# Optimization experiments

Measured on AMD Instinct MI355X. Metric: run time of the kernel, lower is better.

## Reference

```python
import jax, jax.numpy as jnp
import numpy as np


def _forward(agent_qs, ally_states, enemy_states, W_al, b_al, W_en, b_en, Wq, bq, Wk, bk,
             w1_W1, w1_b1, w1_W2, w1_b2, wf_W1, wf_b1, wf_W2, wf_b2, hb_W, hb_b,
             v_W1, v_b1, v_W2, v_b2):
    A, B, S, _ = ally_states.shape
    E = A + enemy_states.shape[0]
    D = W_al.shape[1]
    Da = Wq.shape[1]
    # entity encoders: [A,B,S,D], [En,B,S,D]
    ally_embed = ally_states @ W_al + b_al
    enemy_embed = enemy_states @ W_en + b_en
    entity = jnp.concatenate([ally_embed, enemy_embed], axis=0)      # [E,B,S,D]
    ent_bs = jnp.transpose(entity, (1, 2, 0, 3))                     # [B,S,E,D]
    q = ent_bs @ Wq + bq                                             # [B,S,E,Da]
    k = ent_bs @ Wk + bk                                             # [B,S,E,Da]
    scale = jnp.asarray(Da, q.dtype) ** 0.5
    energy = jnp.einsum('bsid,bsjd->bsij', q / scale, k)             # [B,S,E,E]
    # torch softmax(dim=1) on [BS,E,E] == softmax over the query axis i
    attn = jax.nn.softmax(energy, axis=2)
    # bmm(value[BS,D,E], attn).mean(-1) == value @ mean_j attn[:, :, e, j]
    attn_mean = jnp.mean(attn, axis=3)                               # [B,S,E]
    attn_out = jnp.einsum('bsed,bse->bsd', ent_bs, attn_mean)        # [B,S,D]
    ally_bs = jnp.transpose(ally_embed, (1, 2, 0, 3))                # [B,S,A,D]
    emi = jnp.concatenate(
        [jnp.broadcast_to(attn_out[:, :, None, :], (B, S, A, D)), ally_bs], axis=-1)  # [B,S,A,2D]
    # hypernets (2-layer)
    w1 = jnp.abs(jax.nn.relu(emi @ w1_W1 + w1_b1) @ w1_W2 + w1_b2)   # [B,S,A,M]
    b1 = attn_out @ hb_W + hb_b                                      # [B,S,M]
    hidden = jax.nn.elu(jnp.einsum('bsa,bsam->bsm', agent_qs, w1) + b1)
    wf = jnp.abs(jax.nn.relu(attn_out @ wf_W1 + wf_b1) @ wf_W2 + wf_b2)  # [B,S,M]
    v = jax.nn.relu(attn_out @ v_W1 + v_b1) @ v_W2 + v_b2            # [B,S,1]
    q_tot = jnp.einsum('bsm,bsm->bs', hidden, wf)[..., None] + v     # [B,S,1]
    return q_tot


def setup_inputs() -> dict:
    key = jax.random.key(0)
    B, S, A, En = 128, 128, 8, 8
    NFal, NFen, D, Da, M, H = 32, 16, 64, 128, 32, 64
    ks = jax.random.split(key, 32)
    p = lambda i, shape: jax.random.normal(ks[i], shape, dtype=jnp.float32) * 0.05
    return dict(
        agent_qs=jax.random.normal(ks[0], (B, S, A), dtype=jnp.float32),
        ally_states=jax.random.normal(ks[1], (A, B, S, NFal), dtype=jnp.float32),
        enemy_states=jax.random.normal(ks[2], (En, B, S, NFen), dtype=jnp.float32),
        W_al=p(3, (NFal, D)), b_al=p(4, (D,)), W_en=p(5, (NFen, D)), b_en=p(6, (D,)),
        Wq=p(7, (D, Da)), bq=p(8, (Da,)), Wk=p(9, (D, Da)), bk=p(10, (Da,)),
        w1_W1=p(11, (2 * D, H)), w1_b1=p(12, (H,)), w1_W2=p(13, (H, M)), w1_b2=p(14, (M,)),
        wf_W1=p(15, (D, H)), wf_b1=p(16, (H,)), wf_W2=p(17, (H, M)), wf_b2=p(18, (M,)),
        hb_W=p(19, (D, M)), hb_b=p(20, (M,)),
        v_W1=p(21, (D, M)), v_b1=p(22, (M,)), v_W2=p(23, (M, 1)), v_b2=p(24, (1,)),
    )


def reference(agent_qs, ally_states, enemy_states, W_al, b_al, W_en, b_en, Wq, bq, Wk, bk,
              w1_W1, w1_b1, w1_W2, w1_b2, wf_W1, wf_b1, wf_W2, wf_b2, hb_W, hb_b,
              v_W1, v_b1, v_W2, v_b2):
    return _forward(agent_qs, ally_states, enemy_states, W_al, b_al, W_en, b_en, Wq, bq, Wk, bk,
                    w1_W1, w1_b1, w1_W2, w1_b2, wf_W1, wf_b1, wf_W2, wf_b2, hb_W, hb_b,
                    v_W1, v_b1, v_W2, v_b2)
```

## Files before the change

### kernel.cpp

```cpp
#include <hip/hip_runtime.h>
#include <hip/hip_bf16.h>


#define B_   128
#define S_   128
#define BS_  (B_ * S_)
#define WPB  2
#define INV_S 0.08838834764831845f

typedef short bs8 __attribute__((ext_vector_type(8)));
typedef float f4  __attribute__((ext_vector_type(4)));

#define MFMA(a, b, c) __builtin_amdgcn_mfma_f32_16x16x32_bf16((a), (b), (c), 0, 0, 0)
#define LOADB(t) (*(const bs8*)&fb[(size_t)(t) * 512 + lane * 8])

__device__ __forceinline__ short f2bf(float f) {
    union { float f; unsigned u; } v; v.f = f;
    unsigned r = v.u + 0x7fffu + ((v.u >> 16) & 1u);
    return (short)(r >> 16);
}

__global__ __launch_bounds__(64)
void qmix_pre1(const float* __restrict__ Wq, const float* __restrict__ Wk,
               const float* __restrict__ bk,
               float* __restrict__ Ms, float* __restrict__ vq)
{
    const int blk = blockIdx.x, t = threadIdx.x;
    float p;
    if (blk < 4096) {
        const int k = blk >> 6, n = blk & 63;
        p = Wq[k * 128 + t] * Wk[n * 128 + t]
          + Wq[k * 128 + 64 + t] * Wk[n * 128 + 64 + t];
        #pragma unroll
        for (int off = 32; off >= 1; off >>= 1) p += __shfl_down(p, off, 64);
        if (t == 0) Ms[k * 64 + n] = p * INV_S;
    } else {
        const int d = blk - 4096;
        p = Wq[d * 128 + t] * bk[t] + Wq[d * 128 + 64 + t] * bk[64 + t];
        #pragma unroll
        for (int off = 32; off >= 1; off >>= 1) p += __shfl_down(p, off, 64);
        if (t == 0) vq[d] = p * INV_S;
    }
}

__global__ __launch_bounds__(64)
void qmix_pack(const float* __restrict__ Ms,
               const float* __restrict__ W_al, const float* __restrict__ W_en,
               const float* __restrict__ w1_W1, const float* __restrict__ w1_W2,
               const float* __restrict__ vq,
               short* __restrict__ fb)
{
    const int blk = blockIdx.x, lane = threadIdx.x;
    const int quad = lane >> 4, l16 = lane & 15;
    bs8 v;
    if (blk < 8) {
        const int ks = blk >> 2, n = (blk & 3) * 16 + l16;
        #pragma unroll
        for (int j = 0; j < 8; ++j)
            v[j] = f2bf(Ms[(ks * 32 + quad * 8 + j) * 64 + n]);
    } else if (blk < 16) {
        const bool en = (blk >= 12);
        const float* W = en ? W_en : W_al;
        const int Krows = en ? 16 : 32;
        const int n = ((blk - (en ? 12 : 8)) & 3) * 16 + l16;
        #pragma unroll
        for (int j = 0; j < 8; ++j) {
            const int k = quad * 8 + j;
            v[j] = (k < Krows) ? f2bf(W[k * 64 + n]) : (short)0;
        }
    } else if (blk < 32) {
        const int t = blk - 16, ks = t >> 2, n = (t & 3) * 16 + l16;
        #pragma unroll
        for (int j = 0; j < 8; ++j)
            v[j] = f2bf(w1_W1[(ks * 32 + quad * 8 + j) * 64 + n]);
    } else if (blk < 36) {
        const int t = blk - 32, ks = t >> 1, n = (t & 1) * 16 + l16;
        #pragma unroll
        for (int j = 0; j < 8; ++j)
            v[j] = f2bf(w1_W2[(ks * 32 + quad * 8 + j) * 32 + n]);
    } else {
        const int ks = blk - 36;
        #pragma unroll
        for (int j = 0; j < 8; ++j)
            v[j] = (l16 == 0) ? f2bf(vq[ks * 32 + quad * 8 + j]) : (short)0;
    }
    *(bs8*)&fb[(size_t)blk * 512 + lane * 8] = v;
}

struct __align__(16) WaveLds {
    short entb[16][72];
    short scr[16][72];
    float aoutf[64];
    short aoutb[64];
    float h[64];
    float qs[8];
};

__global__ __launch_bounds__(64 * WPB)
void qmix_main(const float* __restrict__ agent_qs,
               const float* __restrict__ ally, const float* __restrict__ enemy,
               const float* __restrict__ b_al, const float* __restrict__ b_en,
               const float* __restrict__ w1_b1, const float* __restrict__ w1_b2,
               const float* __restrict__ wf_W1, const float* __restrict__ wf_b1,
               const float* __restrict__ wf_W2, const float* __restrict__ wf_b2,
               const float* __restrict__ hb_W,  const float* __restrict__ hb_b,
               const float* __restrict__ v_W1,  const float* __restrict__ v_b1,
               const float* __restrict__ v_W2,  const float* __restrict__ v_b2,
               const short* __restrict__ fb,
               float* __restrict__ out)
{
    const int w    = threadIdx.x >> 6;
    const int lane = threadIdx.x & 63;
    const int site = blockIdx.x * WPB + w;
    const int quad = lane >> 4, l16 = lane & 15;

    __shared__ WaveLds lds[WPB];
    WaveLds& L = lds[w];

    if (lane < 8) L.qs[lane] = agent_qs[(size_t)site * 8 + lane];

    bs8 a_al = {0,0,0,0,0,0,0,0}, a_en = {0,0,0,0,0,0,0,0};
    if (l16 < 8) {
        const float* pa = ally + ((size_t)l16 * BS_ + site) * 32 + quad * 8;
        const float4 f0 = *(const float4*)pa, f1 = *(const float4*)(pa + 4);
        a_al[0]=f2bf(f0.x); a_al[1]=f2bf(f0.y); a_al[2]=f2bf(f0.z); a_al[3]=f2bf(f0.w);
        a_al[4]=f2bf(f1.x); a_al[5]=f2bf(f1.y); a_al[6]=f2bf(f1.z); a_al[7]=f2bf(f1.w);
    } else if (quad < 2) {
        const float* pe = enemy + ((size_t)(l16 - 8) * BS_ + site) * 16 + quad * 8;
        const float4 f0 = *(const float4*)pe, f1 = *(const float4*)(pe + 4);
        a_en[0]=f2bf(f0.x); a_en[1]=f2bf(f0.y); a_en[2]=f2bf(f0.z); a_en[3]=f2bf(f0.w);
        a_en[4]=f2bf(f1.x); a_en[5]=f2bf(f1.y); a_en[6]=f2bf(f1.z); a_en[7]=f2bf(f1.w);
    }

    f4 encf[4];
    #pragma unroll
    for (int n0t = 0; n0t < 4; ++n0t) {
        f4 acc = {0.f, 0.f, 0.f, 0.f};
        acc = MFMA(a_al, LOADB(8 + n0t), acc);
        acc = MFMA(a_en, LOADB(12 + n0t), acc);
        const int d = n0t * 16 + l16;
        const float bal = b_al[d], ben = b_en[d];
        #pragma unroll
        for (int r = 0; r < 4; ++r) {
            const int row = quad * 4 + r;
            const float v = acc[r] + (row < 8 ? bal : ben);
            encf[n0t][r] = v;
            L.entb[row][d] = f2bf(v);
        }
    }
    __syncthreads();

    const bs8 ae0 = *(const bs8*)&L.entb[l16][quad * 8];
    const bs8 ae1 = *(const bs8*)&L.entb[l16][32 + quad * 8];
    f4 pqacc = {0.f, 0.f, 0.f, 0.f};
    pqacc = MFMA(ae0, LOADB(36), pqacc);
    pqacc = MFMA(ae1, LOADB(37), pqacc);
    #pragma unroll
    for (int n0t = 0; n0t < 4; ++n0t) {
        f4 acc = {0.f, 0.f, 0.f, 0.f};
        acc = MFMA(ae0, LOADB(0 + n0t), acc);
        acc = MFMA(ae1, LOADB(4 + n0t), acc);
        const int d = n0t * 16 + l16;
        #pragma unroll
        for (int r = 0; r < 4; ++r) L.scr[quad * 4 + r][d] = f2bf(acc[r]);
    }
    __syncthreads();

    f4 eacc = {0.f, 0.f, 0.f, 0.f};
    {
        const bs8 at0 = *(const bs8*)&L.scr[l16][quad * 8];
        const bs8 at1 = *(const bs8*)&L.scr[l16][32 + quad * 8];
        eacc = MFMA(at0, ae0, eacc);
        eacc = MFMA(at1, ae1, eacc);
        const int src = lane & 48;
        #pragma unroll
        for (int r = 0; r < 4; ++r) eacc[r] += __shfl(pqacc[r], src, 64);
    }

    float amean_r[4];
    {
        float cmax = fmaxf(fmaxf(eacc[0], eacc[1]), fmaxf(eacc[2], eacc[3]));
        cmax = fmaxf(cmax, __shfl_xor(cmax, 16, 64));
        cmax = fmaxf(cmax, __shfl_xor(cmax, 32, 64));
        float er[4], csum = 0.f;
        #pragma unroll
        for (int r = 0; r < 4; ++r) { er[r] = __expf(eacc[r] - cmax); csum += er[r]; }
        csum += __shfl_xor(csum, 16, 64);
        csum += __shfl_xor(csum, 32, 64);
        const float inv = 1.f / csum;
        #pragma unroll
        for (int r = 0; r < 4; ++r) {
            float p = er[r] * inv;
            p += __shfl_xor(p, 1, 64);
            p += __shfl_xor(p, 2, 64);
            p += __shfl_xor(p, 4, 64);
            p += __shfl_xor(p, 8, 64);
            amean_r[r] = p * (1.f / 16.f);
        }
    }

    #pragma unroll
    for (int n0t = 0; n0t < 4; ++n0t) {
        float ap = amean_r[0] * encf[n0t][0] + amean_r[1] * encf[n0t][1]
                 + amean_r[2] * encf[n0t][2] + amean_r[3] * encf[n0t][3];
        ap += __shfl_xor(ap, 16, 64);
        ap += __shfl_xor(ap, 32, 64);
        if (quad == 0) {
            L.aoutf[n0t * 16 + l16] = ap;
            L.aoutb[n0t * 16 + l16] = f2bf(ap);
        }
    }
    __syncthreads();

    float b1m = 0.f, hvp = 0.f;
    {
        const float* Wx = (lane < 32) ? (hb_W + lane) : (v_W1 + (lane - 32));
        float acc_wf = wf_b1[lane];
        float acc_x  = (lane < 32) ? hb_b[lane] : v_b1[lane - 32];
        #pragma unroll 4
        for (int d4 = 0; d4 < 16; ++d4) {
            const int r = d4 * 4;
            const float4 av = *(const float4*)&L.aoutf[r];
            acc_wf += av.x * wf_W1[(r + 0) * 64 + lane] + av.y * wf_W1[(r + 1) * 64 + lane]
                    + av.z * wf_W1[(r + 2) * 64 + lane] + av.w * wf_W1[(r + 3) * 64 + lane];
            acc_x  += av.x * Wx[(r + 0) * 32] + av.y * Wx[(r + 1) * 32]
                    + av.z * Wx[(r + 2) * 32] + av.w * Wx[(r + 3) * 32];
        }
        L.h[lane] = fmaxf(acc_wf, 0.f);
        if (lane < 32) b1m = acc_x;
        else           hvp = fmaxf(acc_x, 0.f) * v_W2[lane - 32];
    }
    const float hvx = __shfl_xor(hvp, 32, 64);
    __syncthreads();

    float wfm = 0.f;
    if (lane < 32) {
        float a2 = wf_b2[lane];
        #pragma unroll 4
        for (int t4 = 0; t4 < 16; ++t4) {
            const int r = t4 * 4;
            const float4 h4 = *(const float4*)&L.h[r];
            a2 += h4.x * wf_W2[(r + 0) * 32 + lane] + h4.y * wf_W2[(r + 1) * 32 + lane]
                + h4.z * wf_W2[(r + 2) * 32 + lane] + h4.w * wf_W2[(r + 3) * 32 + lane];
        }
        wfm = fabsf(a2);
    }

    {
        const bs8 a0 = *(const bs8*)&L.aoutb[quad * 8];
        const bs8 a1 = *(const bs8*)&L.aoutb[32 + quad * 8];
        f4 hacc[4];
        #pragma unroll
        for (int n0t = 0; n0t < 4; ++n0t) {
            f4 acc = {0.f, 0.f, 0.f, 0.f};
            acc = MFMA(a0,  LOADB(16 + 0 + n0t), acc);
            acc = MFMA(a1,  LOADB(16 + 4 + n0t), acc);
            acc = MFMA(ae0, LOADB(16 + 8 + n0t), acc);
            acc = MFMA(ae1, LOADB(16 + 12 + n0t), acc);
            hacc[n0t] = acc;
        }
        #pragma unroll
        for (int n0t = 0; n0t < 4; ++n0t) {
            const int d = n0t * 16 + l16;
            const float b1v = w1_b1[d];
            #pragma unroll
            for (int r = 0; r < 4; ++r) {
                const int row = quad * 4 + r;
                if (row < 8)
                    L.scr[row][d] = f2bf(fmaxf(hacc[n0t][r] + b1v, 0.f));
            }
        }
    }
    __syncthreads();

    float p0 = 0.f, p1 = 0.f;
    {
        const bs8 ah0 = *(const bs8*)&L.scr[l16][quad * 8];
        const bs8 ah1 = *(const bs8*)&L.scr[l16][32 + quad * 8];
        #pragma unroll
        for (int n0t = 0; n0t < 2; ++n0t) {
            f4 acc = {0.f, 0.f, 0.f, 0.f};
            acc = MFMA(ah0, LOADB(32 + 0 + n0t), acc);
            acc = MFMA(ah1, LOADB(32 + 2 + n0t), acc);
            const int col = n0t * 16 + l16;
            const float b2v = w1_b2[col];
            float p = 0.f;
            if (quad < 2) {
                #pragma unroll
                for (int r = 0; r < 4; ++r)
                    p += L.qs[quad * 4 + r] * fabsf(acc[r] + b2v);
            }
            if (n0t == 0) p0 = p; else p1 = p;
        }
        p0 += __shfl_xor(p0, 16, 64);
        p1 += __shfl_xor(p1, 16, 64);
    }

    float contrib = 0.f;
    if (lane < 32) {
        float hp = (lane < 16 ? p0 : p1) + b1m;
        hp = (hp > 0.f) ? hp : (__expf(hp) - 1.f);
        contrib = hp * wfm + hvx;
    }
    #pragma unroll
    for (int off = 16; off >= 1; off >>= 1)
        contrib += __shfl_down(contrib, off, 64);
    if (lane == 0) out[site] = contrib + v_b2[0];
}

extern "C" void kernel_launch(void* const* d_in, const int* in_sizes, int n_in,
                              void* d_out, int out_size, void* d_ws, size_t ws_size,
                              hipStream_t stream) {
    const float* p[25];
    for (int i = 0; i < 25; ++i) p[i] = (const float*)d_in[i];
    short* fb = (short*)d_ws;
    float* vq = (float*)((char*)d_ws + 38 * 512 * 2);
    float* Ms = vq + 64;

    qmix_pre1<<<4096 + 64, 64, 0, stream>>>(p[7], p[9], p[10], Ms, vq);
    qmix_pack<<<38, 64, 0, stream>>>(Ms, p[3], p[5], p[11], p[13], vq, fb);
    qmix_main<<<BS_ / WPB, 64 * WPB, 0, stream>>>(
        p[0], p[1], p[2], p[4], p[6], p[12], p[14],
        p[15], p[16], p[17], p[18], p[19], p[20], p[21], p[22], p[23], p[24],
        fb, (float*)d_out);
}
```

Measured before the change: 173.0 us.

## Move hypernet small GEMVs onto bf16 MFMA with prepacked weight fragments

The per-site scalar fp32 GEMVs for the wf, hb and v hypernets, which read weights from global memory lane by lane, are replaced by bf16 MFMA tiles. The weights are prepacked into the fragment buffer by the pack kernel, which grows from 38 to 58 blocks. The kernel also adds an occupancy hint to the launch bounds and shrinks the per-wave LDS footprint. This cuts per-lane global loads and FMA loops, but lowers these paths from fp32 to bf16 precision and wastes most of each MFMA, since only one row holds useful data.

```diff
diff --git a/kernel.cpp b/kernel.cpp
--- a/kernel.cpp
+++ b/kernel.cpp
@@ -48,6 +48,8 @@
                const float* __restrict__ W_al, const float* __restrict__ W_en,
                const float* __restrict__ w1_W1, const float* __restrict__ w1_W2,
                const float* __restrict__ vq,
+               const float* __restrict__ wf_W1, const float* __restrict__ hb_W,
+               const float* __restrict__ v_W1,  const float* __restrict__ wf_W2,
                short* __restrict__ fb)
 {
     const int blk = blockIdx.x, lane = threadIdx.x;
@@ -78,11 +80,27 @@
         #pragma unroll
         for (int j = 0; j < 8; ++j)
             v[j] = f2bf(w1_W2[(ks * 32 + quad * 8 + j) * 32 + n]);
+    } else if (blk < 38) {
+        const int ks = blk - 36;
+        #pragma unroll
+        for (int j = 0; j < 8; ++j)
+            v[j] = (l16 == 0) ? f2bf(vq[ks * 32 + quad * 8 + j]) : (short)0;
+    } else if (blk < 54) {
+        const int t = blk - 38, ks = t >> 3, n = (t & 7) * 16 + l16;
+        #pragma unroll
+        for (int j = 0; j < 8; ++j) {
+            const int k = ks * 32 + quad * 8 + j;
+            float w;
+            if (n < 64)       w = wf_W1[k * 64 + n];
+            else if (n < 96)  w = hb_W[k * 32 + (n - 64)];
+            else              w = v_W1[k * 32 + (n - 96)];
+            v[j] = f2bf(w);
+        }
     } else {
-        const int ks = blk - 36;
-        #pragma unroll
-        for (int j = 0; j < 8; ++j)
-            v[j] = (l16 == 0) ? f2bf(vq[ks * 32 + quad * 8 + j]) : (short)0;
+        const int t = blk - 54, ks = t >> 1, n = (t & 1) * 16 + l16;
+        #pragma unroll
+        for (int j = 0; j < 8; ++j)
+            v[j] = f2bf(wf_W2[(ks * 32 + quad * 8 + j) * 32 + n]);
     }
     *(bs8*)&fb[(size_t)blk * 512 + lane * 8] = v;
 }
@@ -90,21 +108,18 @@
 struct __align__(16) WaveLds {
     short entb[16][72];
     short scr[16][72];
-    float aoutf[64];
     short aoutb[64];
-    float h[64];
+    short hb16[64];
     float qs[8];
 };
 
-__global__ __launch_bounds__(64 * WPB)
+__global__ __launch_bounds__(64 * WPB, 4)
 void qmix_main(const float* __restrict__ agent_qs,
                const float* __restrict__ ally, const float* __restrict__ enemy,
                const float* __restrict__ b_al, const float* __restrict__ b_en,
                const float* __restrict__ w1_b1, const float* __restrict__ w1_b2,
-               const float* __restrict__ wf_W1, const float* __restrict__ wf_b1,
-               const float* __restrict__ wf_W2, const float* __restrict__ wf_b2,
-               const float* __restrict__ hb_W,  const float* __restrict__ hb_b,
-               const float* __restrict__ v_W1,  const float* __restrict__ v_b1,
+               const float* __restrict__ wf_b1, const float* __restrict__ wf_b2,
+               const float* __restrict__ hb_b,  const float* __restrict__ v_b1,
                const float* __restrict__ v_W2,  const float* __restrict__ v_b2,
                const short* __restrict__ fb,
                float* __restrict__ out)
@@ -205,70 +220,68 @@
                  + amean_r[2] * encf[n0t][2] + amean_r[3] * encf[n0t][3];
         ap += __shfl_xor(ap, 16, 64);
         ap += __shfl_xor(ap, 32, 64);
-        if (quad == 0) {
-            L.aoutf[n0t * 16 + l16] = ap;
-            L.aoutb[n0t * 16 + l16] = f2bf(ap);
-        }
-    }
-    __syncthreads();
-
-    float b1m = 0.f, hvp = 0.f;
-    {
-        const float* Wx = (lane < 32) ? (hb_W + lane) : (v_W1 + (lane - 32));
-        float acc_wf = wf_b1[lane];
-        float acc_x  = (lane < 32) ? hb_b[lane] : v_b1[lane - 32];
-        #pragma unroll 4
-        for (int d4 = 0; d4 < 16; ++d4) {
-            const int r = d4 * 4;
-            const float4 av = *(const float4*)&L.aoutf[r];
-            acc_wf += av.x * wf_W1[(r + 0) * 64 + lane] + av.y * wf_W1[(r + 1) * 64 + lane]
-                    + av.z * wf_W1[(r + 2) * 64 + lane] + av.w * wf_W1[(r + 3) * 64 + lane];
-            acc_x  += av.x * Wx[(r + 0) * 32] + av.y * Wx[(r + 1) * 32]
-                    + av.z * Wx[(r + 2) * 32] + av.w * Wx[(r + 3) * 32];
-        }
-        L.h[lane] = fmaxf(acc_wf, 0.f);
-        if (lane < 32) b1m = acc_x;
-        else           hvp = fmaxf(acc_x, 0.f) * v_W2[lane - 32];
-    }
-    const float hvx = __shfl_xor(hvp, 32, 64);
-    __syncthreads();
-
-    float wfm = 0.f;
-    if (lane < 32) {
-        float a2 = wf_b2[lane];
-        #pragma unroll 4
-        for (int t4 = 0; t4 < 16; ++t4) {
-            const int r = t4 * 4;
-            const float4 h4 = *(const float4*)&L.h[r];
-            a2 += h4.x * wf_W2[(r + 0) * 32 + lane] + h4.y * wf_W2[(r + 1) * 32 + lane]
-                + h4.z * wf_W2[(r + 2) * 32 + lane] + h4.w * wf_W2[(r + 3) * 32 + lane];
-        }
-        wfm = fabsf(a2);
-    }
-
-    {
-        const bs8 a0 = *(const bs8*)&L.aoutb[quad * 8];
-        const bs8 a1 = *(const bs8*)&L.aoutb[32 + quad * 8];
-        f4 hacc[4];
-        #pragma unroll
-        for (int n0t = 0; n0t < 4; ++n0t) {
-            f4 acc = {0.f, 0.f, 0.f, 0.f};
-            acc = MFMA(a0,  LOADB(16 + 0 + n0t), acc);
-            acc = MFMA(a1,  LOADB(16 + 4 + n0t), acc);
-            acc = MFMA(ae0, LOADB(16 + 8 + n0t), acc);
-            acc = MFMA(ae1, LOADB(16 + 12 + n0t), acc);
-            hacc[n0t] = acc;
-        }
-        #pragma unroll
-        for (int n0t = 0; n0t < 4; ++n0t) {
-            const int d = n0t * 16 + l16;
-            const float b1v = w1_b1[d];
-            #pragma unroll
-            for (int r = 0; r < 4; ++r) {
-                const int row = quad * 4 + r;
-                if (row < 8)
-                    L.scr[row][d] = f2bf(fmaxf(hacc[n0t][r] + b1v, 0.f));
-            }
+        if (quad == 0) L.aoutb[n0t * 16 + l16] = f2bf(ap);
+    }
+    __syncthreads();
+
+    const bs8 a0 = *(const bs8*)&L.aoutb[quad * 8];
+    const bs8 a1 = *(const bs8*)&L.aoutb[32 + quad * 8];
+
+    float x[8];
+    #pragma unroll
+    for (int n0t = 0; n0t < 8; ++n0t) {
+        f4 acc = {0.f, 0.f, 0.f, 0.f};
+        acc = MFMA(a0, LOADB(38 + n0t), acc);
+        acc = MFMA(a1, LOADB(46 + n0t), acc);
+        x[n0t] = acc[0];
+    }
+    {
+        const float xh = (quad == 0) ? x[0] : (quad == 1) ? x[1]
+                       : (quad == 2) ? x[2] : x[3];
+        L.hb16[lane] = f2bf(fmaxf(xh + wf_b1[lane], 0.f));
+    }
+    const float b1m = ((lane < 16) ? x[4] : x[5]) + ((lane < 32) ? hb_b[lane] : 0.f);
+    float vsum;
+    {
+        float hv = fmaxf(x[6] + v_b1[l16], 0.f)      * v_W2[l16]
+                 + fmaxf(x[7] + v_b1[16 + l16], 0.f) * v_W2[16 + l16];
+        hv += __shfl_xor(hv, 1, 64);
+        hv += __shfl_xor(hv, 2, 64);
+        hv += __shfl_xor(hv, 4, 64);
+        hv += __shfl_xor(hv, 8, 64);
+        vsum = hv;
+    }
+    __syncthreads();
+
+    float wfm;
+    {
+        const bs8 h0 = *(const bs8*)&L.hb16[quad * 8];
+        const bs8 h1 = *(const bs8*)&L.hb16[32 + quad * 8];
+        f4 acc0 = {0.f, 0.f, 0.f, 0.f};
+        acc0 = MFMA(h0, LOADB(54), acc0);
+        acc0 = MFMA(h1, LOADB(56), acc0);
+        f4 acc1 = {0.f, 0.f, 0.f, 0.f};
+        acc1 = MFMA(h0, LOADB(55), acc1);
+        acc1 = MFMA(h1, LOADB(57), acc1);
+        const float w0 = fabsf(acc0[0] + wf_b2[l16]);
+        const float w1 = fabsf(acc1[0] + wf_b2[16 + l16]);
+        wfm = (lane < 16) ? w0 : w1;
+    }
+
+    #pragma unroll
+    for (int n0t = 0; n0t < 4; ++n0t) {
+        f4 acc = {0.f, 0.f, 0.f, 0.f};
+        acc = MFMA(a0,  LOADB(16 + 0 + n0t), acc);
+        acc = MFMA(a1,  LOADB(16 + 4 + n0t), acc);
+        acc = MFMA(ae0, LOADB(16 + 8 + n0t), acc);
+        acc = MFMA(ae1, LOADB(16 + 12 + n0t), acc);
+        const int d = n0t * 16 + l16;
+        const float b1v = w1_b1[d];
+        #pragma unroll
+        for (int r = 0; r < 4; ++r) {
+            const int row = quad * 4 + r;
+            if (row < 8)
+                L.scr[row][d] = f2bf(fmaxf(acc[r] + b1v, 0.f));
         }
     }
     __syncthreads();
@@ -300,12 +313,12 @@
     if (lane < 32) {
         float hp = (lane < 16 ? p0 : p1) + b1m;
         hp = (hp > 0.f) ? hp : (__expf(hp) - 1.f);
-        contrib = hp * wfm + hvx;
+        contrib = hp * wfm;
     }
     #pragma unroll
     for (int off = 16; off >= 1; off >>= 1)
         contrib += __shfl_down(contrib, off, 64);
-    if (lane == 0) out[site] = contrib + v_b2[0];
+    if (lane == 0) out[site] = contrib + vsum + v_b2[0];
 }
 
 extern "C" void kernel_launch(void* const* d_in, const int* in_sizes, int n_in,
@@ -314,13 +327,14 @@
     const float* p[25];
     for (int i = 0; i < 25; ++i) p[i] = (const float*)d_in[i];
     short* fb = (short*)d_ws;
-    float* vq = (float*)((char*)d_ws + 38 * 512 * 2);
+    float* vq = (float*)((char*)d_ws + 58 * 512 * 2);
     float* Ms = vq + 64;
 
     qmix_pre1<<<4096 + 64, 64, 0, stream>>>(p[7], p[9], p[10], Ms, vq);
-    qmix_pack<<<38, 64, 0, stream>>>(Ms, p[3], p[5], p[11], p[13], vq, fb);
+    qmix_pack<<<58, 64, 0, stream>>>(Ms, p[3], p[5], p[11], p[13], vq,
+                                     p[15], p[19], p[21], p[17], fb);
     qmix_main<<<BS_ / WPB, 64 * WPB, 0, stream>>>(
         p[0], p[1], p[2], p[4], p[6], p[12], p[14],
-        p[15], p[16], p[17], p[18], p[19], p[20], p[21], p[22], p[23], p[24],
+        p[16], p[18], p[20], p[22], p[23], p[24],
         fb, (float*)d_out);
 }
```

New measurement: 163.2 us. -5.6%, faster.
